# Kernel optimization log

Hardware: AMD Instinct MI355X
Metric: run time of the kernel (lower is better)

Reference implementation:

```python
import jax, jax.numpy as jnp
import numpy as np

N = 100000   # nodes
E = 1600000  # edges
G = 2048     # graphs in batch
NC = 204     # n_classes
DEPTH = 5
EPS = 1e-5


def setup_inputs() -> dict:
    key = jax.random.key(0)
    ks = jax.random.split(key, 20)
    rn = lambda k, s, sc=0.05: (jax.random.normal(k, s, jnp.float32) * sc)
    inp = {
        "h": jax.random.normal(ks[0], (N, 78), jnp.float32),
        "edge_src": jax.random.randint(ks[1], (E,), 0, N),
        "edge_dst": jax.random.randint(ks[2], (E,), 0, N),
        "graph_ids": jnp.sort(jax.random.randint(ks[3], (N,), 0, G)),
        "W1": rn(ks[4], (78, 128)),
        "b1": rn(ks[5], (128,)),
        "g1_gamma": jnp.ones((128,), jnp.float32),
        "g1_beta": jnp.zeros((128,), jnp.float32),
        "Wg": rn(ks[6], (DEPTH - 1, 128, 128)),
        "bg": rn(ks[7], (DEPTH - 1, 128)),
        "g_gamma": jnp.ones((DEPTH - 1, 128), jnp.float32),
        "g_beta": jnp.zeros((DEPTH - 1, 128), jnp.float32),
        "fc1_W": rn(ks[8], (128, 512)),
        "fc1_b": rn(ks[9], (512,)),
        "bn1_gamma": jnp.ones((512,), jnp.float32),
        "bn1_beta": jnp.zeros((512,), jnp.float32),
        "lin_W": rn(ks[10], (512, 256)),
        "lin_b": rn(ks[11], (256,)),
        "lbn_gamma": jnp.ones((256,), jnp.float32),
        "lbn_beta": jnp.zeros((256,), jnp.float32),
        "fc2_W": rn(ks[12], (256, 408)),
        "fc2_b": rn(ks[13], (408,)),
    }
    return inp


def _bn(x, gamma, beta):
    # torch BatchNorm1d training-mode normalization: biased batch var, eps=1e-5
    mu = jnp.mean(x, axis=0)
    var = jnp.var(x, axis=0)
    return (x - mu) * jax.lax.rsqrt(var + EPS) * gamma + beta


def _gin(h, src, dst, W, b):
    # DGL GINConv (eps=0, sum agg): apply_func(h + sum_neigh(h)); module adds apply_func(h)
    agg = jax.ops.segment_sum(h[src], dst, num_segments=h.shape[0])  # [N, d]
    return (h + agg) @ W + b + (h @ W + b)


def reference(h, edge_src, edge_dst, graph_ids, W1, b1, g1_gamma, g1_beta,
              Wg, bg, g_gamma, g_beta, fc1_W, fc1_b, bn1_gamma, bn1_beta,
              lin_W, lin_b, lbn_gamma, lbn_beta, fc2_W, fc2_b):
    x = jax.nn.relu(_bn(_gin(h, edge_src, edge_dst, W1, b1), g1_gamma, g1_beta))
    for i in range(DEPTH - 1):
        x = jax.nn.relu(_bn(_gin(x, edge_src, edge_dst, Wg[i], bg[i]),
                            g_gamma[i], g_beta[i]))
    # sum readout over nodes of each graph -> [G, 128]
    xg = jax.ops.segment_sum(x, graph_ids, num_segments=G)
    x = jax.nn.relu(_bn(xg @ fc1_W + fc1_b, bn1_gamma, bn1_beta))
    x = jax.nn.relu(_bn(x @ lin_W + lin_b, lbn_gamma, lbn_beta))
    logits = x @ fc2_W + fc2_b          # [G, 2*NC]
    return jax.nn.sigmoid(logits[:, -NC:])  # [G, NC]
```

## Files before the change

kernel.cpp:

```cpp
#include <hip/hip_runtime.h>
#include <hip/hip_fp16.h>
#include <math.h>

#define N_NODES 100000
#define N_EDGES 1600000
#define N_GRAPHS 2048
#define NCLS 204
#define EPS_BN 1e-5f
#define NBUCK ((N_NODES + 255) / 256)
#define BIN_CHUNK 8192

typedef __attribute__((ext_vector_type(8))) _Float16 f16x8;
typedef __attribute__((ext_vector_type(4))) float f32x4;

__device__ __forceinline__ uint pack2h(float a, float b) {
  __half2 h = __floats2half2_rn(a, b);
  return *reinterpret_cast<uint*>(&h);
}
__device__ __forceinline__ float2 unpack2h(uint u) {
  __half2 h = *reinterpret_cast<__half2*>(&u);
  return __half22float2(h);
}
__device__ __forceinline__ ushort f2h(float v) {
  __half h = __float2half_rn(v);
  return *reinterpret_cast<ushort*>(&h);
}

__global__ __launch_bounds__(256) void k_bin_count(const int* __restrict__ dst,
                                                   int* __restrict__ bcnt, int E) {
  __shared__ int hist[NBUCK];
  int t = threadIdx.x;
  int e0 = blockIdx.x * BIN_CHUNK;
  for (int b = t; b < NBUCK; b += 256) hist[b] = 0;
  __syncthreads();
  for (int e = e0 + t; e < min(e0 + BIN_CHUNK, E); e += 256)
    atomicAdd(&hist[dst[e] >> 8], 1);
  __syncthreads();
  for (int b = t; b < NBUCK; b += 256)
    if (hist[b] > 0) atomicAdd(&bcnt[b], hist[b]);
}

__global__ __launch_bounds__(512) void k_bucket_scan(const int* __restrict__ bcnt,
                                                     int* __restrict__ bbase,
                                                     int* __restrict__ bcur) {
  __shared__ int sh[512];
  int t = threadIdx.x;
  int v = (t < NBUCK) ? bcnt[t] : 0;
  sh[t] = v;
  __syncthreads();
  for (int d = 1; d < 512; d <<= 1) {
    int x = (t >= d) ? sh[t - d] : 0;
    __syncthreads();
    sh[t] += x;
    __syncthreads();
  }
  if (t < NBUCK) {
    bbase[t + 1] = sh[t];
    bcur[t] = sh[t] - v;
    if (t == 0) bbase[0] = 0;
  }
}

__global__ __launch_bounds__(256) void k_bin(const int* __restrict__ src,
                                             const int* __restrict__ dst,
                                             int* __restrict__ cursor,
                                             uint* __restrict__ staging, int E) {
  __shared__ int hist[NBUCK];
  __shared__ int base_s[NBUCK];
  int t = threadIdx.x;
  int e0 = blockIdx.x * BIN_CHUNK;
  for (int b = t; b < NBUCK; b += 256) hist[b] = 0;
  __syncthreads();
  for (int e = e0 + t; e < min(e0 + BIN_CHUNK, E); e += 256)
    atomicAdd(&hist[dst[e] >> 8], 1);
  __syncthreads();
  for (int b = t; b < NBUCK; b += 256) {
    int hh = hist[b];
    if (hh > 0) base_s[b] = atomicAdd(&cursor[b], hh);
    hist[b] = 0;
  }
  __syncthreads();
  for (int e = e0 + t; e < min(e0 + BIN_CHUNK, E); e += 256) {
    int d = dst[e];
    int b = d >> 8;
    int r = atomicAdd(&hist[b], 1);
    staging[base_s[b] + r] = (uint)src[e] | ((uint)(d & 255) << 24);
  }
}

__global__ __launch_bounds__(256) void k_place2(const uint* __restrict__ staging,
                                                const int* __restrict__ bbase,
                                                int* __restrict__ row_ptr,
                                                uint* __restrict__ csrb, int nNodes, int E) {
  __shared__ int cnt[256];
  __shared__ int scn[256];
  __shared__ int cur[256];
  int t = threadIdx.x;
  int b = blockIdx.x;
  int n0 = b * 256;
  cnt[t] = 0;
  __syncthreads();
  int s = bbase[b], e = bbase[b + 1];
  for (int i = s + t; i < e; i += 256) atomicAdd(&cnt[staging[i] >> 24], 1);
  __syncthreads();
  int v = cnt[t];
  scn[t] = v;
  __syncthreads();
  for (int d = 1; d < 256; d <<= 1) {
    int x = (t >= d) ? scn[t - d] : 0;
    __syncthreads();
    scn[t] += x;
    __syncthreads();
  }
  int excl = scn[t] - v;
  if (n0 + t < nNodes) row_ptr[n0 + t] = s + excl;
  cur[t] = s + excl;
  __syncthreads();
  for (int i = s + t; i < e; i += 256) {
    uint ed = staging[i];
    int pos = atomicAdd(&cur[ed >> 24], 1);
    csrb[pos] = (ed & 0xFFFFFF) << 8;
  }
  if (b == 0 && t == 0) row_ptr[nNodes] = E;
}

__global__ void k_conv_h(const float* __restrict__ h, uint* __restrict__ hb, int nNodes) {
  int i = blockIdx.x * blockDim.x + threadIdx.x;
  if (i < nNodes * 64) {
    int n = i >> 6, cp = i & 63;
    int c = cp * 2;
    float a = (c < 78) ? h[(size_t)n * 78 + c] : 0.0f;
    float b = (c + 1 < 78) ? h[(size_t)n * 78 + c + 1] : 0.0f;
    hb[i] = pack2h(a, b);
  }
}

__global__ void k_prep_wt_all(const float* __restrict__ W1, const float* __restrict__ Wg,
                              ushort* __restrict__ Wt) {
  int i = blockIdx.x * blockDim.x + threadIdx.x;
  int layer = blockIdx.y;
  if (i < 128 * 128) {
    int n = i >> 7, k = i & 127;
    const float* W = (layer == 0) ? W1 : Wg + (size_t)(layer - 1) * 128 * 128;
    int K = (layer == 0) ? 78 : 128;
    float v = (k < K) ? W[(size_t)k * 128 + n] : 0.0f;
    Wt[(size_t)layer * 128 * 128 + i] = f2h(v);
  }
}

__global__ void k_prep_wt_gen(const float* __restrict__ W, int wld, int col_off, int nkeep,
                              int K, ushort* __restrict__ Wt, int total) {
  int i = blockIdx.x * blockDim.x + threadIdx.x;
  if (i < total) {
    int n = i / K, k = i - n * K;
    float v = (n < nkeep) ? W[(size_t)k * wld + col_off + n] : 0.0f;
    Wt[i] = f2h(v);
  }
}

__global__ __launch_bounds__(256) void k_act(const uint* __restrict__ y,
                                             const float* __restrict__ psum,
                                             const float* __restrict__ psq,
                                             const float* __restrict__ pgamma,
                                             const float* __restrict__ pbeta,
                                             float invM,
                                             uint* __restrict__ xact, int total) {
  int i = blockIdx.x * blockDim.x + threadIdx.x;
  if (i < total) {
    int c0 = (i & 63) * 2, c1 = c0 + 1;
    float mu0 = psum[c0] * invM;
    float A0 = pgamma[c0] * rsqrtf(psq[c0] * invM - mu0 * mu0 + EPS_BN);
    float B0 = pbeta[c0] - mu0 * A0;
    float mu1 = psum[c1] * invM;
    float A1 = pgamma[c1] * rsqrtf(psq[c1] * invM - mu1 * mu1 + EPS_BN);
    float B1 = pbeta[c1] - mu1 * A1;
    float2 f = unpack2h(y[i]);
    xact[i] = pack2h(fmaxf(f.x * A0 + B0, 0.f), fmaxf(f.y * A1 + B1, 0.f));
  }
}

__global__ __launch_bounds__(256) void k_agg(const char* __restrict__ xraw,
                                             const int* __restrict__ row_ptr,
                                             const uint* __restrict__ csrb,
                                             char* __restrict__ Mraw, int nNodes) {
  int n = blockIdx.x * 4 + (threadIdx.x >> 6);
  if (n >= nNodes) return;
  int l = threadIdx.x & 63;
  int slot = l >> 4;
  int ch16 = l & 15;
  int coff = ch16 * 16;

  float acc[8];
#pragma unroll
  for (int k = 0; k < 8; k++) acc[k] = 0.f;

  auto accum = [&](uint4 v) {
    float2 f0 = unpack2h(v.x), f1 = unpack2h(v.y), f2 = unpack2h(v.z), f3 = unpack2h(v.w);
    acc[0] += f0.x; acc[1] += f0.y;
    acc[2] += f1.x; acc[3] += f1.y;
    acc[4] += f2.x; acc[5] += f2.y;
    acc[6] += f3.x; acc[7] += f3.y;
  };

  if (slot == 0) {
    uint4 v = *reinterpret_cast<const uint4*>(xraw + (size_t)n * 256 + coff);
    float2 f0 = unpack2h(v.x), f1 = unpack2h(v.y), f2 = unpack2h(v.z), f3 = unpack2h(v.w);
    acc[0] = 2.f * f0.x; acc[1] = 2.f * f0.y;
    acc[2] = 2.f * f1.x; acc[3] = 2.f * f1.y;
    acc[4] = 2.f * f2.x; acc[5] = 2.f * f2.y;
    acc[6] = 2.f * f3.x; acc[7] = 2.f * f3.y;
  }

  int s = row_ptr[n], e = row_ptr[n + 1];
  for (int base = s; base < e; base += 64) {
    int cnt = e - base;
    if (cnt > 64) cnt = 64;
    uint myoff = (base + l < e) ? csrb[base + l] : 0;
    int nfull = cnt >> 2;
    for (int j = 0; j < nfull; j++) {
      uint off = __shfl(myoff, 4 * j + slot);
      uint4 v = *reinterpret_cast<const uint4*>(xraw + (size_t)off + coff);
      accum(v);
    }
    int jj = nfull * 4 + slot;
    uint off = __shfl(myoff, jj < 64 ? jj : 63);
    if (jj < cnt) {
      uint4 v = *reinterpret_cast<const uint4*>(xraw + (size_t)off + coff);
      accum(v);
    }
  }

#pragma unroll
  for (int k = 0; k < 8; k++) {
    acc[k] += __shfl_xor(acc[k], 16);
    acc[k] += __shfl_xor(acc[k], 32);
  }
  if (slot == 0) {
    uint4 o;
    o.x = pack2h(acc[0], acc[1]);
    o.y = pack2h(acc[2], acc[3]);
    o.z = pack2h(acc[4], acc[5]);
    o.w = pack2h(acc[6], acc[7]);
    *reinterpret_cast<uint4*>(Mraw + (size_t)n * 256 + coff) = o;
  }
}

#define SWZ(row, boff) ((boff) ^ (((row) & 7) << 4))
__global__ __launch_bounds__(256) void k_gemm_mfma(const ushort* __restrict__ A,
                                                   const ushort* __restrict__ Wt,
                                                   const float* __restrict__ bias, float bscale,
                                                   ushort* __restrict__ Y, int Mrows,
                                                   float* __restrict__ gsum,
                                                   float* __restrict__ gsq) {
  __shared__ ushort As[128 * 128];
  __shared__ ushort Bs[128 * 128];
  __shared__ float sred[4][128], qred[4][128];
  int t = threadIdx.x;
  int r0 = blockIdx.x * 128;
  char* Ab = (char*)As;
  char* Bb = (char*)Bs;

  for (int it = 0; it < 8; it++) {
    int e = it * 256 + t;
    int row = e >> 4, seg = e & 15;
    uint4 va = make_uint4(0, 0, 0, 0);
    int gr = r0 + row;
    if (gr < Mrows) va = *reinterpret_cast<const uint4*>(A + (size_t)gr * 128 + seg * 8);
    *reinterpret_cast<uint4*>(Ab + row * 256 + SWZ(row, seg * 16)) = va;
    uint4 vb = *reinterpret_cast<const uint4*>(Wt + (size_t)row * 128 + seg * 8);
    *reinterpret_cast<uint4*>(Bb + row * 256 + SWZ(row, seg * 16)) = vb;
  }
  __syncthreads();

  int wi = t >> 6;
  int l = t & 63;
  int lr = l & 15;
  int kp = l >> 4;

  f32x4 acc[2][8];
#pragma unroll
  for (int mi = 0; mi < 2; mi++)
#pragma unroll
    for (int ni = 0; ni < 8; ni++) acc[mi][ni] = (f32x4){0.f, 0.f, 0.f, 0.f};

#pragma unroll
  for (int ki = 0; ki < 4; ki++) {
    f16x8 a[2], b[8];
#pragma unroll
    for (int mi = 0; mi < 2; mi++) {
      int row = wi * 32 + mi * 16 + lr;
      a[mi] = *reinterpret_cast<const f16x8*>(Ab + row * 256 + SWZ(row, ki * 64 + kp * 16));
    }
#pragma unroll
    for (int ni = 0; ni < 8; ni++) {
      int row = ni * 16 + lr;
      b[ni] = *reinterpret_cast<const f16x8*>(Bb + row * 256 + SWZ(row, ki * 64 + kp * 16));
    }
#pragma unroll
    for (int mi = 0; mi < 2; mi++)
#pragma unroll
      for (int ni = 0; ni < 8; ni++)
        acc[mi][ni] = __builtin_amdgcn_mfma_f32_16x16x32_f16(a[mi], b[ni], acc[mi][ni], 0, 0, 0);
  }

  float s_part[8], q_part[8];
#pragma unroll
  for (int ni = 0; ni < 8; ni++) { s_part[ni] = 0.f; q_part[ni] = 0.f; }

#pragma unroll
  for (int mi = 0; mi < 2; mi++) {
    int rbase = r0 + wi * 32 + mi * 16 + kp * 4;
#pragma unroll
    for (int ni = 0; ni < 8; ni++) {
      int col = ni * 16 + lr;
      float bb = bscale * bias[col];
#pragma unroll
      for (int j = 0; j < 4; j++) {
        int r = rbase + j;
        if (r < Mrows) {
          float yv = acc[mi][ni][j] + bb;
          Y[(size_t)r * 128 + col] = f2h(yv);
          s_part[ni] += yv;
          q_part[ni] += yv * yv;
        }
      }
    }
  }

#pragma unroll
  for (int ni = 0; ni < 8; ni++) {
    s_part[ni] += __shfl_xor(s_part[ni], 16, 64);
    s_part[ni] += __shfl_xor(s_part[ni], 32, 64);
    q_part[ni] += __shfl_xor(q_part[ni], 16, 64);
    q_part[ni] += __shfl_xor(q_part[ni], 32, 64);
  }
  if (kp == 0) {
#pragma unroll
    for (int ni = 0; ni < 8; ni++) {
      sred[wi][ni * 16 + lr] = s_part[ni];
      qred[wi][ni * 16 + lr] = q_part[ni];
    }
  }
  __syncthreads();
  if (t < 128) {
    float S = sred[0][t] + sred[1][t] + sred[2][t] + sred[3][t];
    float Q = qred[0][t] + qred[1][t] + qred[2][t] + qred[3][t];
    atomicAdd(&gsum[t], S);
    atomicAdd(&gsq[t], Q);
  }
}

template <int AMODE, int OMODE>
__global__ __launch_bounds__(256) void k_head_mfma(const void* __restrict__ Aptr,
                                                   int Mrows, int K,
                                                   const ushort* __restrict__ Wt,
                                                   const float* __restrict__ bias,
                                                   int col_off, int ncols,
                                                   const float* __restrict__ nAc,
                                                   const float* __restrict__ nBc,
                                                   void* __restrict__ Yout, int Nld,
                                                   float* __restrict__ gsum,
                                                   float* __restrict__ gsq) {
  __shared__ ushort As[128 * 128];
  __shared__ ushort Bs[128 * 128];
  __shared__ float sred[4][128], qred[4][128];
  int t = threadIdx.x;
  int r0 = blockIdx.y * 128;
  int c0 = blockIdx.x * 128;
  char* Ab = (char*)As;
  char* Bb = (char*)Bs;

  int wi = t >> 6;
  int l = t & 63;
  int lr = l & 15;
  int kp = l >> 4;

  f32x4 acc[2][8];
#pragma unroll
  for (int mi = 0; mi < 2; mi++)
#pragma unroll
    for (int ni = 0; ni < 8; ni++) acc[mi][ni] = (f32x4){0.f, 0.f, 0.f, 0.f};

  for (int k0 = 0; k0 < K; k0 += 128) {
    if (k0) __syncthreads();
    for (int it = 0; it < 8; it++) {
      int e = it * 256 + t;
      int row = e >> 4, seg = e & 15;
      int gr = r0 + row;
      uint4 va;
      if (AMODE == 0) {
        const float* Af = (const float*)Aptr;
        float4 f0 = {0.f, 0.f, 0.f, 0.f}, f1 = {0.f, 0.f, 0.f, 0.f};
        if (gr < Mrows) {
          f0 = *reinterpret_cast<const float4*>(Af + (size_t)gr * K + k0 + seg * 8);
          f1 = *reinterpret_cast<const float4*>(Af + (size_t)gr * K + k0 + seg * 8 + 4);
        }
        va.x = pack2h(f0.x, f0.y); va.y = pack2h(f0.z, f0.w);
        va.z = pack2h(f1.x, f1.y); va.w = pack2h(f1.z, f1.w);
      } else {
        const uint* Au = (const uint*)Aptr;
        uint4 r4 = make_uint4(0, 0, 0, 0);
        if (gr < Mrows) r4 = *reinterpret_cast<const uint4*>(Au + (size_t)gr * (K >> 1) + ((k0 + seg * 8) >> 1));
        int c = k0 + seg * 8;
        uint uu[4] = {r4.x, r4.y, r4.z, r4.w};
#pragma unroll
        for (int q = 0; q < 4; q++) {
          float2 f = unpack2h(uu[q]);
          float aa = fmaxf(f.x * nAc[c + 2 * q] + nBc[c + 2 * q], 0.f);
          float bb = fmaxf(f.y * nAc[c + 2 * q + 1] + nBc[c + 2 * q + 1], 0.f);
          uu[q] = pack2h(aa, bb);
        }
        va = make_uint4(uu[0], uu[1], uu[2], uu[3]);
      }
      *reinterpret_cast<uint4*>(Ab + row * 256 + SWZ(row, seg * 16)) = va;
      uint4 vb = *reinterpret_cast<const uint4*>(Wt + (size_t)(c0 + row) * K + k0 + seg * 8);
      *reinterpret_cast<uint4*>(Bb + row * 256 + SWZ(row, seg * 16)) = vb;
    }
    __syncthreads();

#pragma unroll
    for (int ki = 0; ki < 4; ki++) {
      f16x8 a[2], b[8];
#pragma unroll
      for (int mi = 0; mi < 2; mi++) {
        int row = wi * 32 + mi * 16 + lr;
        a[mi] = *reinterpret_cast<const f16x8*>(Ab + row * 256 + SWZ(row, ki * 64 + kp * 16));
      }
#pragma unroll
      for (int ni = 0; ni < 8; ni++) {
        int row = ni * 16 + lr;
        b[ni] = *reinterpret_cast<const f16x8*>(Bb + row * 256 + SWZ(row, ki * 64 + kp * 16));
      }
#pragma unroll
      for (int mi = 0; mi < 2; mi++)
#pragma unroll
        for (int ni = 0; ni < 8; ni++)
          acc[mi][ni] = __builtin_amdgcn_mfma_f32_16x16x32_f16(a[mi], b[ni], acc[mi][ni], 0, 0, 0);
    }
  }

  if (OMODE == 0) {
    float s_part[8], q_part[8];
#pragma unroll
    for (int ni = 0; ni < 8; ni++) { s_part[ni] = 0.f; q_part[ni] = 0.f; }
#pragma unroll
    for (int mi = 0; mi < 2; mi++) {
      int rbase = r0 + wi * 32 + mi * 16 + kp * 4;
#pragma unroll
      for (int ni = 0; ni < 8; ni++) {
        int gc = c0 + ni * 16 + lr;
        float bb = bias[col_off + gc];
#pragma unroll
        for (int j = 0; j < 4; j++) {
          int r = rbase + j;
          if (r < Mrows) {
            float yv = acc[mi][ni][j] + bb;
            ((ushort*)Yout)[(size_t)r * Nld + gc] = f2h(yv);
            s_part[ni] += yv;
            q_part[ni] += yv * yv;
          }
        }
      }
    }
#pragma unroll
    for (int ni = 0; ni < 8; ni++) {
      s_part[ni] += __shfl_xor(s_part[ni], 16, 64);
      s_part[ni] += __shfl_xor(s_part[ni], 32, 64);
      q_part[ni] += __shfl_xor(q_part[ni], 16, 64);
      q_part[ni] += __shfl_xor(q_part[ni], 32, 64);
    }
    if (kp == 0) {
#pragma unroll
      for (int ni = 0; ni < 8; ni++) {
        sred[wi][ni * 16 + lr] = s_part[ni];
        qred[wi][ni * 16 + lr] = q_part[ni];
      }
    }
    __syncthreads();
    if (t < 128) {
      float S = sred[0][t] + sred[1][t] + sred[2][t] + sred[3][t];
      float Q = qred[0][t] + qred[1][t] + qred[2][t] + qred[3][t];
      atomicAdd(&gsum[c0 + t], S);
      atomicAdd(&gsq[c0 + t], Q);
    }
  } else {
#pragma unroll
    for (int mi = 0; mi < 2; mi++) {
      int rbase = r0 + wi * 32 + mi * 16 + kp * 4;
#pragma unroll
      for (int ni = 0; ni < 8; ni++) {
        int gc = c0 + ni * 16 + lr;
        if (gc < ncols) {
          float bb = bias[col_off + gc];
#pragma unroll
          for (int j = 0; j < 4; j++) {
            int r = rbase + j;
            if (r < Mrows) {
              float v = acc[mi][ni][j] + bb;
              ((float*)Yout)[(size_t)r * Nld + gc] = 1.0f / (1.0f + expf(-v));
            }
          }
        }
      }
    }
  }
}

__global__ void k_bnparams(const float* __restrict__ sum, const float* __restrict__ sumsq,
                           const float* __restrict__ gamma, const float* __restrict__ beta,
                           float* __restrict__ Ac, float* __restrict__ Bc,
                           int C, float invM) {
  int c = blockIdx.x * blockDim.x + threadIdx.x;
  if (c < C) {
    float mu = sum[c] * invM;
    float var = sumsq[c] * invM - mu * mu;
    float rs = rsqrtf(var + EPS_BN);
    float a = gamma[c] * rs;
    Ac[c] = a;
    Bc[c] = beta[c] - mu * a;
  }
}

__global__ __launch_bounds__(64) void k_readout(const uint* __restrict__ y,
                                                const int* __restrict__ gid,
                                                const float* __restrict__ psum,
                                                const float* __restrict__ psq,
                                                const float* __restrict__ pgamma,
                                                const float* __restrict__ pbeta,
                                                float invM,
                                                float* __restrict__ xg, int nNodes) {
  int l = threadIdx.x;
  int n0 = blockIdx.x * 64;
  int n1 = min(n0 + 64, nNodes);
  if (n0 >= nNodes) return;
  int c0 = 2 * l, c1 = 2 * l + 1;
  float mu0 = psum[c0] * invM;
  float va0 = psq[c0] * invM - mu0 * mu0;
  float A0 = pgamma[c0] * rsqrtf(va0 + EPS_BN);
  float B0 = pbeta[c0] - mu0 * A0;
  float mu1 = psum[c1] * invM;
  float va1 = psq[c1] * invM - mu1 * mu1;
  float A1 = pgamma[c1] * rsqrtf(va1 + EPS_BN);
  float B1 = pbeta[c1] - mu1 * A1;
  float a0 = 0, a1 = 0;
  int cur = gid[n0];
  for (int n = n0; n < n1; n++) {
    int g = gid[n];
    if (g != cur) {
      atomicAdd(&xg[(size_t)cur * 128 + 2 * l], a0);
      atomicAdd(&xg[(size_t)cur * 128 + 2 * l + 1], a1);
      a0 = 0; a1 = 0; cur = g;
    }
    float2 f = unpack2h(y[(size_t)n * 64 + l]);
    a0 += fmaxf(f.x * A0 + B0, 0.f);
    a1 += fmaxf(f.y * A1 + B1, 0.f);
  }
  atomicAdd(&xg[(size_t)cur * 128 + 2 * l], a0);
  atomicAdd(&xg[(size_t)cur * 128 + 2 * l + 1], a1);
}

extern "C" void kernel_launch(void* const* d_in, const int* in_sizes, int n_in,
                              void* d_out, int out_size, void* d_ws, size_t ws_size,
                              hipStream_t stream) {
  const float* h    = (const float*)d_in[0];
  const int*   esrc = (const int*)d_in[1];
  const int*   edst = (const int*)d_in[2];
  const int*   gid  = (const int*)d_in[3];
  const float* W1   = (const float*)d_in[4];
  const float* b1   = (const float*)d_in[5];
  const float* g1g  = (const float*)d_in[6];
  const float* g1b  = (const float*)d_in[7];
  const float* Wg   = (const float*)d_in[8];
  const float* bg   = (const float*)d_in[9];
  const float* gg   = (const float*)d_in[10];
  const float* gb   = (const float*)d_in[11];
  const float* fc1W = (const float*)d_in[12];
  const float* fc1b = (const float*)d_in[13];
  const float* bn1g = (const float*)d_in[14];
  const float* bn1b = (const float*)d_in[15];
  const float* linW = (const float*)d_in[16];
  const float* linb = (const float*)d_in[17];
  const float* lbng = (const float*)d_in[18];
  const float* lbnb = (const float*)d_in[19];
  const float* fc2W = (const float*)d_in[20];
  const float* fc2b = (const float*)d_in[21];
  float* out = (float*)d_out;

  char* p = (char*)d_ws;
  auto alloc = [&](size_t bytes) {
    char* q = p;
    p += (bytes + 255) & ~(size_t)255;
    return q;
  };
  int* row_ptr = (int*)alloc((N_NODES + 1) * sizeof(int));
  int* bcnt    = (int*)alloc(NBUCK * sizeof(int));
  int* bbase   = (int*)alloc((NBUCK + 1) * sizeof(int));
  int* bcur    = (int*)alloc(NBUCK * sizeof(int));
  uint* csrb   = (uint*)alloc(N_EDGES * sizeof(uint));
  uint* hb     = (uint*)alloc((size_t)N_NODES * 64 * sizeof(uint));
  uint* Mb     = (uint*)alloc((size_t)N_NODES * 64 * sizeof(uint));
  uint* yb     = (uint*)alloc((size_t)N_NODES * 64 * sizeof(uint));
  uint* xact   = (uint*)alloc((size_t)N_NODES * 64 * sizeof(uint));
  ushort* Wt   = (ushort*)alloc(5 * 128 * 128 * sizeof(ushort));
  ushort* fc1Wt = (ushort*)alloc(512 * 128 * sizeof(ushort));
  ushort* linWt = (ushort*)alloc(256 * 512 * sizeof(ushort));
  ushort* fc2Wt = (ushort*)alloc(256 * 256 * sizeof(ushort));
  float* stats = (float*)alloc(2816 * sizeof(float));
  float* Ac    = (float*)alloc(512 * sizeof(float));
  float* Bc    = (float*)alloc(512 * sizeof(float));
  float* xg    = (float*)alloc((size_t)N_GRAPHS * 128 * sizeof(float));
  uint* y1b    = (uint*)alloc((size_t)N_GRAPHS * 256 * sizeof(uint));
  uint* y2b    = (uint*)alloc((size_t)N_GRAPHS * 128 * sizeof(uint));
  uint* staging = (uint*)Mb;

  float* lsum = stats;
  float* fsum1 = stats + 1280;
  float* fsq1  = stats + 1792;
  float* lsum2 = stats + 2304;
  float* lsq2  = stats + 2560;

  k_conv_h<<<(N_NODES * 64 + 255) / 256, 256, 0, stream>>>(h, hb, N_NODES);
  {
    dim3 g(64, 5);
    k_prep_wt_all<<<g, 256, 0, stream>>>(W1, Wg, Wt);
  }
  k_prep_wt_gen<<<(512 * 128 + 255) / 256, 256, 0, stream>>>(fc1W, 512, 0, 512, 128, fc1Wt, 512 * 128);
  k_prep_wt_gen<<<(256 * 512 + 255) / 256, 256, 0, stream>>>(linW, 256, 0, 256, 512, linWt, 256 * 512);
  k_prep_wt_gen<<<(256 * 256 + 255) / 256, 256, 0, stream>>>(fc2W, 408, 204, 204, 256, fc2Wt, 256 * 256);

  hipMemsetAsync(stats, 0, 2816 * sizeof(float), stream);
  hipMemsetAsync(xg, 0, (size_t)N_GRAPHS * 128 * sizeof(float), stream);

  hipMemsetAsync(bcnt, 0, NBUCK * sizeof(int), stream);
  k_bin_count<<<(N_EDGES + BIN_CHUNK - 1) / BIN_CHUNK, 256, 0, stream>>>(edst, bcnt, N_EDGES);
  k_bucket_scan<<<1, 512, 0, stream>>>(bcnt, bbase, bcur);
  k_bin<<<(N_EDGES + BIN_CHUNK - 1) / BIN_CHUNK, 256, 0, stream>>>(esrc, edst, bcur,
                                                                   staging, N_EDGES);
  k_place2<<<NBUCK, 256, 0, stream>>>(staging, bbase, row_ptr, csrb, N_NODES, N_EDGES);

  const float invN = 1.0f / (float)N_NODES;
  const float invG = 1.0f / (float)N_GRAPHS;

  for (int layer = 0; layer < 5; layer++) {
    const ushort* Wl = Wt + (size_t)layer * 128 * 128;
    const float* bl  = (layer == 0) ? b1 : bg + (size_t)(layer - 1) * 128;
    const float* gl  = (layer == 0) ? g1g : gg + (size_t)(layer - 1) * 128;
    const float* bl2 = (layer == 0) ? g1b : gb + (size_t)(layer - 1) * 128;
    float* st = lsum + (size_t)layer * 256;

    const char* xin = (layer == 0) ? (const char*)hb : (const char*)xact;
    k_agg<<<(N_NODES + 3) / 4, 256, 0, stream>>>(xin, row_ptr, csrb, (char*)Mb, N_NODES);
    k_gemm_mfma<<<(N_NODES + 127) / 128, 256, 0, stream>>>((const ushort*)Mb, Wl, bl, 2.0f,
                                                           (ushort*)yb, N_NODES,
                                                           st, st + 128);
    if (layer < 4)
      k_act<<<(N_NODES * 64 + 255) / 256, 256, 0, stream>>>(yb, st, st + 128, gl, bl2,
                                                            invN, xact, N_NODES * 64);
  }

  k_readout<<<(N_NODES + 63) / 64, 64, 0, stream>>>(yb, gid,
                                                    lsum + 4 * 256, lsum + 4 * 256 + 128,
                                                    gg + 3 * 128, gb + 3 * 128, invN,
                                                    xg, N_NODES);

  k_head_mfma<0, 0><<<dim3(4, 16), 256, 0, stream>>>(xg, N_GRAPHS, 128, fc1Wt, fc1b, 0, 512,
                                                     nullptr, nullptr, y1b, 512, fsum1, fsq1);
  k_bnparams<<<1, 512, 0, stream>>>(fsum1, fsq1, bn1g, bn1b, Ac, Bc, 512, invG);

  k_head_mfma<1, 0><<<dim3(2, 16), 256, 0, stream>>>(y1b, N_GRAPHS, 512, linWt, linb, 0, 256,
                                                     Ac, Bc, y2b, 256, lsum2, lsq2);
  k_bnparams<<<1, 256, 0, stream>>>(lsum2, lsq2, lbng, lbnb, Ac, Bc, 256, invG);

  k_head_mfma<1, 1><<<dim3(2, 16), 256, 0, stream>>>(y2b, N_GRAPHS, 256, fc2Wt, fc2b, 204, NCLS,
                                                     Ac, Bc, out, NCLS, nullptr, nullptr);
}
```

Baseline: 716.9 us.

## Fuse BN+ReLU activation into neighbor aggregation, recomputing per gathered row

Removes the separate k_act pass and the xact buffer. The aggregation kernel now reads the raw fp16 GEMM output, builds the BN scale and shift for its two channels, and applies BN+ReLU in half precision to every gathered neighbor row before summing. The gather is also restructured so each lane reads one 4-byte channel pair per edge across all 64 lanes, instead of 16-byte chunks split over four edge slots. This saves one full read and write pass per layer, at the cost of redoing the normalization on every edge gather and doing that math in fp16.

```diff
diff --git a/kernel.cpp b/kernel.cpp
--- a/kernel.cpp
+++ b/kernel.cpp
@@ -158,91 +158,92 @@
   }
 }
 
-__global__ __launch_bounds__(256) void k_act(const uint* __restrict__ y,
-                                             const float* __restrict__ psum,
-                                             const float* __restrict__ psq,
-                                             const float* __restrict__ pgamma,
-                                             const float* __restrict__ pbeta,
-                                             float invM,
-                                             uint* __restrict__ xact, int total) {
-  int i = blockIdx.x * blockDim.x + threadIdx.x;
-  if (i < total) {
-    int c0 = (i & 63) * 2, c1 = c0 + 1;
+__global__ void k_bnparams(const float* __restrict__ sum, const float* __restrict__ sumsq,
+                           const float* __restrict__ gamma, const float* __restrict__ beta,
+                           float* __restrict__ Ac, float* __restrict__ Bc,
+                           int C, float invM) {
+  int c = blockIdx.x * blockDim.x + threadIdx.x;
+  if (c < C) {
+    float mu = sum[c] * invM;
+    float var = sumsq[c] * invM - mu * mu;
+    float rs = rsqrtf(var + EPS_BN);
+    float a = gamma[c] * rs;
+    Ac[c] = a;
+    Bc[c] = beta[c] - mu * a;
+  }
+}
+
+template <bool NRM>
+__global__ __launch_bounds__(256) void k_agg_f(const uint* __restrict__ y,
+                                               const int* __restrict__ row_ptr,
+                                               const uint* __restrict__ csrb,
+                                               const float* __restrict__ psum,
+                                               const float* __restrict__ psq,
+                                               const float* __restrict__ pgamma,
+                                               const float* __restrict__ pbeta,
+                                               float invM,
+                                               uint* __restrict__ M, int nNodes) {
+  int n = blockIdx.x * 4 + (threadIdx.x >> 6);
+  if (n >= nNodes) return;
+  int l = threadIdx.x & 63;
+  int loff = l * 4;
+  const char* yraw = (const char*)y;
+
+  __half2 An, Bn;
+  if (NRM) {
+    int c0 = 2 * l, c1 = c0 + 1;
     float mu0 = psum[c0] * invM;
     float A0 = pgamma[c0] * rsqrtf(psq[c0] * invM - mu0 * mu0 + EPS_BN);
     float B0 = pbeta[c0] - mu0 * A0;
     float mu1 = psum[c1] * invM;
     float A1 = pgamma[c1] * rsqrtf(psq[c1] * invM - mu1 * mu1 + EPS_BN);
     float B1 = pbeta[c1] - mu1 * A1;
-    float2 f = unpack2h(y[i]);
-    xact[i] = pack2h(fmaxf(f.x * A0 + B0, 0.f), fmaxf(f.y * A1 + B1, 0.f));
-  }
-}
-
-__global__ __launch_bounds__(256) void k_agg(const char* __restrict__ xraw,
-                                             const int* __restrict__ row_ptr,
-                                             const uint* __restrict__ csrb,
-                                             char* __restrict__ Mraw, int nNodes) {
-  int n = blockIdx.x * 4 + (threadIdx.x >> 6);
-  if (n >= nNodes) return;
-  int l = threadIdx.x & 63;
-  int slot = l >> 4;
-  int ch16 = l & 15;
-  int coff = ch16 * 16;
-
-  float acc[8];
-#pragma unroll
-  for (int k = 0; k < 8; k++) acc[k] = 0.f;
-
-  auto accum = [&](uint4 v) {
-    float2 f0 = unpack2h(v.x), f1 = unpack2h(v.y), f2 = unpack2h(v.z), f3 = unpack2h(v.w);
-    acc[0] += f0.x; acc[1] += f0.y;
-    acc[2] += f1.x; acc[3] += f1.y;
-    acc[4] += f2.x; acc[5] += f2.y;
-    acc[6] += f3.x; acc[7] += f3.y;
+    An = __floats2half2_rn(A0, A1);
+    Bn = __floats2half2_rn(B0, B1);
+  }
+  const __half2 z2 = __floats2half2_rn(0.f, 0.f);
+
+  auto fval = [&](uint v) -> float2 {
+    __half2 hv = *reinterpret_cast<__half2*>(&v);
+    if (NRM) {
+      hv = __hfma2(hv, An, Bn);
+      hv = __hmul2(hv, __hgt2(hv, z2));
+    }
+    return __half22float2(hv);
   };
 
-  if (slot == 0) {
-    uint4 v = *reinterpret_cast<const uint4*>(xraw + (size_t)n * 256 + coff);
-    float2 f0 = unpack2h(v.x), f1 = unpack2h(v.y), f2 = unpack2h(v.z), f3 = unpack2h(v.w);
-    acc[0] = 2.f * f0.x; acc[1] = 2.f * f0.y;
-    acc[2] = 2.f * f1.x; acc[3] = 2.f * f1.y;
-    acc[4] = 2.f * f2.x; acc[5] = 2.f * f2.y;
-    acc[6] = 2.f * f3.x; acc[7] = 2.f * f3.y;
-  }
+  uint self = *reinterpret_cast<const uint*>(yraw + (size_t)n * 256 + loff);
+  float2 fs = fval(self);
+  float a0 = 2.f * fs.x, a1 = 2.f * fs.y;
 
   int s = row_ptr[n], e = row_ptr[n + 1];
   for (int base = s; base < e; base += 64) {
     int cnt = e - base;
     if (cnt > 64) cnt = 64;
     uint myoff = (base + l < e) ? csrb[base + l] : 0;
-    int nfull = cnt >> 2;
-    for (int j = 0; j < nfull; j++) {
-      uint off = __shfl(myoff, 4 * j + slot);
-      uint4 v = *reinterpret_cast<const uint4*>(xraw + (size_t)off + coff);
-      accum(v);
-    }
-    int jj = nfull * 4 + slot;
-    uint off = __shfl(myoff, jj < 64 ? jj : 63);
-    if (jj < cnt) {
-      uint4 v = *reinterpret_cast<const uint4*>(xraw + (size_t)off + coff);
-      accum(v);
-    }
-  }
-
-#pragma unroll
-  for (int k = 0; k < 8; k++) {
-    acc[k] += __shfl_xor(acc[k], 16);
-    acc[k] += __shfl_xor(acc[k], 32);
-  }
-  if (slot == 0) {
-    uint4 o;
-    o.x = pack2h(acc[0], acc[1]);
-    o.y = pack2h(acc[2], acc[3]);
-    o.z = pack2h(acc[4], acc[5]);
-    o.w = pack2h(acc[6], acc[7]);
-    *reinterpret_cast<uint4*>(Mraw + (size_t)n * 256 + coff) = o;
-  }
+    int j = 0;
+    for (; j + 4 <= cnt; j += 4) {
+      uint o0 = __shfl(myoff, j);
+      uint o1 = __shfl(myoff, j + 1);
+      uint o2 = __shfl(myoff, j + 2);
+      uint o3 = __shfl(myoff, j + 3);
+      uint v0 = *reinterpret_cast<const uint*>(yraw + (size_t)o0 + loff);
+      uint v1 = *reinterpret_cast<const uint*>(yraw + (size_t)o1 + loff);
+      uint v2 = *reinterpret_cast<const uint*>(yraw + (size_t)o2 + loff);
+      uint v3 = *reinterpret_cast<const uint*>(yraw + (size_t)o3 + loff);
+      float2 f0 = fval(v0), f1 = fval(v1), f2 = fval(v2), f3 = fval(v3);
+      a0 += f0.x + f1.x + f2.x + f3.x;
+      a1 += f0.y + f1.y + f2.y + f3.y;
+    }
+    for (; j < cnt; j++) {
+      uint o = __shfl(myoff, j);
+      uint v = *reinterpret_cast<const uint*>(yraw + (size_t)o + loff);
+      float2 f = fval(v);
+      a0 += f.x;
+      a1 += f.y;
+    }
+  }
+  M[(size_t)n * 64 + l] = pack2h(a0, a1);
 }
 
 #define SWZ(row, boff) ((boff) ^ (((row) & 7) << 4))
@@ -503,21 +504,6 @@
         }
       }
     }
-  }
-}
-
-__global__ void k_bnparams(const float* __restrict__ sum, const float* __restrict__ sumsq,
-                           const float* __restrict__ gamma, const float* __restrict__ beta,
-                           float* __restrict__ Ac, float* __restrict__ Bc,
-                           int C, float invM) {
-  int c = blockIdx.x * blockDim.x + threadIdx.x;
-  if (c < C) {
-    float mu = sum[c] * invM;
-    float var = sumsq[c] * invM - mu * mu;
-    float rs = rsqrtf(var + EPS_BN);
-    float a = gamma[c] * rs;
-    Ac[c] = a;
-    Bc[c] = beta[c] - mu * a;
   }
 }
 
@@ -600,7 +586,6 @@
   uint* hb     = (uint*)alloc((size_t)N_NODES * 64 * sizeof(uint));
   uint* Mb     = (uint*)alloc((size_t)N_NODES * 64 * sizeof(uint));
   uint* yb     = (uint*)alloc((size_t)N_NODES * 64 * sizeof(uint));
-  uint* xact   = (uint*)alloc((size_t)N_NODES * 64 * sizeof(uint));
   ushort* Wt   = (ushort*)alloc(5 * 128 * 128 * sizeof(ushort));
   ushort* fc1Wt = (ushort*)alloc(512 * 128 * sizeof(ushort));
   ushort* linWt = (ushort*)alloc(256 * 512 * sizeof(ushort));
@@ -644,18 +629,22 @@
   for (int layer = 0; layer < 5; layer++) {
     const ushort* Wl = Wt + (size_t)layer * 128 * 128;
     const float* bl  = (layer == 0) ? b1 : bg + (size_t)(layer - 1) * 128;
-    const float* gl  = (layer == 0) ? g1g : gg + (size_t)(layer - 1) * 128;
-    const float* bl2 = (layer == 0) ? g1b : gb + (size_t)(layer - 1) * 128;
+    const float* pg  = (layer == 1) ? g1g : gg + (size_t)(layer - 2) * 128;
+    const float* pb  = (layer == 1) ? g1b : gb + (size_t)(layer - 2) * 128;
     float* st = lsum + (size_t)layer * 256;
 
-    const char* xin = (layer == 0) ? (const char*)hb : (const char*)xact;
-    k_agg<<<(N_NODES + 3) / 4, 256, 0, stream>>>(xin, row_ptr, csrb, (char*)Mb, N_NODES);
+    if (layer == 0)
+      k_agg_f<false><<<(N_NODES + 3) / 4, 256, 0, stream>>>(hb, row_ptr, csrb,
+                                                            nullptr, nullptr, nullptr, nullptr,
+                                                            invN, Mb, N_NODES);
+    else
+      k_agg_f<true><<<(N_NODES + 3) / 4, 256, 0, stream>>>(yb, row_ptr, csrb,
+                                                           lsum + (size_t)(layer - 1) * 256,
+                                                           lsum + (size_t)(layer - 1) * 256 + 128,
+                                                           pg, pb, invN, Mb, N_NODES);
     k_gemm_mfma<<<(N_NODES + 127) / 128, 256, 0, stream>>>((const ushort*)Mb, Wl, bl, 2.0f,
                                                            (ushort*)yb, N_NODES,
                                                            st, st + 128);
-    if (layer < 4)
-      k_act<<<(N_NODES * 64 + 255) / 256, 256, 0, stream>>>(yb, st, st + 128, gl, bl2,
-                                                            invN, xact, N_NODES * 64);
   }
 
   k_readout<<<(N_NODES + 63) / 64, 64, 0, stream>>>(yb, gid,
```

Result: faster. 657.2 us (-8.3%).
